# Optimization experiments

Hardware: AMD Instinct MI355X
Metric: run time of the kernel (lower is better)

The kernel has to match this reference:

```python
import jax, jax.numpy as jnp
import numpy as np

D_MODEL = 1024
N_HEADS = 16
HEAD_DIM = D_MODEL // N_HEADS
INNER = 4 * D_MODEL  # mlp_ratio=4
EPS = 1e-5


def setup_inputs() -> dict:
    key = jax.random.key(0)
    ks = jax.random.split(key, 8)
    B, L = 2, 2048
    s = 0.02
    return {
        "x": jax.random.normal(ks[0], (B, L, D_MODEL), dtype=jnp.float32),
        "w_qkv": jax.random.normal(ks[1], (D_MODEL, 3 * D_MODEL), dtype=jnp.float32) * s,
        "b_qkv": jnp.zeros((3 * D_MODEL,), jnp.float32),
        "w_out": jax.random.normal(ks[2], (D_MODEL, D_MODEL), dtype=jnp.float32) * s,
        "b_out": jnp.zeros((D_MODEL,), jnp.float32),
        "w_fc1": jax.random.normal(ks[3], (D_MODEL, INNER), dtype=jnp.float32) * s,
        "b_fc1": jnp.zeros((INNER,), jnp.float32),
        "w_fc2": jax.random.normal(ks[4], (INNER, D_MODEL), dtype=jnp.float32) * s,
        "b_fc2": jnp.zeros((D_MODEL,), jnp.float32),
        "ln1_g": jnp.ones((D_MODEL,), jnp.float32),
        "ln1_b": jnp.zeros((D_MODEL,), jnp.float32),
        "ln2_g": jnp.ones((D_MODEL,), jnp.float32),
        "ln2_b": jnp.zeros((D_MODEL,), jnp.float32),
    }


def _layernorm(x, g, b):
    mu = jnp.mean(x, axis=-1, keepdims=True)
    var = jnp.mean(jnp.square(x - mu), axis=-1, keepdims=True)
    return (x - mu) * jax.lax.rsqrt(var + EPS) * g + b


def reference(x, w_qkv, b_qkv, w_out, b_out, w_fc1, b_fc1, w_fc2, b_fc2,
              ln1_g, ln1_b, ln2_g, ln2_b):
    B, L, D = x.shape
    scale = HEAD_DIM ** -0.5

    # --- attention (prefill, kv_cache=None, S=L) ---
    h = _layernorm(x, ln1_g, ln1_b)
    qkv = (h @ w_qkv + b_qkv).reshape(B, L, 3, N_HEADS, HEAD_DIM)
    q, k, v = (qkv[:, :, i].transpose(0, 2, 1, 3) for i in range(3))  # (B,H,L,hd)
    attn = jnp.einsum('bhqd,bhkd->bhqk', q, k) * scale
    causal = jnp.arange(L)[None, :] > jnp.arange(L)[:, None]  # col > row
    attn = jnp.where(causal[None, None], -jnp.inf, attn)
    attn = jax.nn.softmax(attn, axis=-1)
    o = jnp.einsum('bhqk,bhkd->bhqd', attn, v).transpose(0, 2, 1, 3).reshape(B, L, D)
    x = x + o @ w_out + b_out

    # --- MLP ---
    h2 = _layernorm(x, ln2_g, ln2_b)
    h2 = jax.nn.gelu(h2 @ w_fc1 + b_fc1, approximate=False)  # torch nn.GELU = exact erf
    x = x + h2 @ w_fc2 + b_fc2
    return x
```

## Files before the change

### kernel.cpp

```cpp
#include <hip/hip_runtime.h>
#include <hip/hip_bf16.h>

typedef unsigned short u16;
typedef unsigned int u32;
typedef short bf16x8 __attribute__((ext_vector_type(8)));
typedef float f32x4 __attribute__((ext_vector_type(4)));

#define LOG2E 1.4426950408889634f

#define SEQ 2048
#define DM 1024
#define NH 16
#define HD 64
#define INNER 4096
#define MTOT 4096
#define QKV_ELEMS 4194304

static __device__ __forceinline__ u16 f2bf(float f) {
  u32 u = __float_as_uint(f);
  u = (u + 0x7fffu + ((u >> 16) & 1u)) >> 16;
  return (u16)u;
}

static __device__ __forceinline__ void async_copy16(void* lds, const void* g) {
  __builtin_amdgcn_global_load_lds(
      (const __attribute__((address_space(1))) u32*)g,
      (__attribute__((address_space(3))) u32*)lds, 16, 0, 0);
}

#define MFMA16(a, b, c) __builtin_amdgcn_mfma_f32_16x16x32_bf16(a, b, c, 0, 0, 0)

__global__ __launch_bounds__(256) void transpose_cast(
    const float* __restrict__ src, u16* __restrict__ dst, int K, int N) {
  __shared__ float tile[32][33];
  int bx = blockIdx.x;
  int by = blockIdx.y;
  int t = threadIdx.x;
  int tr = t >> 5, tc = t & 31;
#pragma unroll
  for (int i = 0; i < 4; ++i) {
    int r = by * 32 + tr + i * 8;
    int c = bx * 32 + tc;
    tile[tr + i * 8][tc] = src[(size_t)r * N + c];
  }
  __syncthreads();
#pragma unroll
  for (int i = 0; i < 4; ++i) {
    int n = bx * 32 + tr + i * 8;
    int kk = by * 32 + tc;
    dst[(size_t)n * K + kk] = f2bf(tile[tc][tr + i * 8]);
  }
}

__global__ __launch_bounds__(256) void ln_kernel(
    const float* __restrict__ x, const float* __restrict__ g,
    const float* __restrict__ b, u16* __restrict__ out) {
  int row = blockIdx.x, t = threadIdx.x;
  const float* xr = x + (size_t)row * DM;
  float4 v = *(const float4*)(xr + t * 4);
  float s = v.x + v.y + v.z + v.w;
  float ss = v.x * v.x + v.y * v.y + v.z * v.z + v.w * v.w;
#pragma unroll
  for (int d = 1; d < 64; d <<= 1) {
    s += __shfl_xor(s, d);
    ss += __shfl_xor(ss, d);
  }
  __shared__ float red[8];
  int w = t >> 6, lane = t & 63;
  if (lane == 0) { red[w] = s; red[4 + w] = ss; }
  __syncthreads();
  s = red[0] + red[1] + red[2] + red[3];
  ss = red[4] + red[5] + red[6] + red[7];
  float mu = s * (1.f / DM);
  float var = ss * (1.f / DM) - mu * mu;
  float rstd = rsqrtf(var + 1e-5f);
  float4 gv = *(const float4*)(g + t * 4);
  float4 bv = *(const float4*)(b + t * 4);
  u32 p0 = (u32)f2bf((v.x - mu) * rstd * gv.x + bv.x) |
           ((u32)f2bf((v.y - mu) * rstd * gv.y + bv.y) << 16);
  u32 p1 = (u32)f2bf((v.z - mu) * rstd * gv.z + bv.z) |
           ((u32)f2bf((v.w - mu) * rstd * gv.w + bv.w) << 16);
  uint2 pk; pk.x = p0; pk.y = p1;
  *(uint2*)(out + (size_t)row * DM + t * 4) = pk;
}

template <int EPI>
__global__ __launch_bounds__(256) void gemm_bt(
    const u16* __restrict__ A, const u16* __restrict__ Bt,
    const float* __restrict__ bias, const float* __restrict__ resid,
    void* __restrict__ outp, int M, int N, int K) {
  __shared__ u16 As[128 * 32];
  __shared__ u16 Bs[128 * 32];
  int t = threadIdx.x;
  int lane = t & 63, w = t >> 6;
  int lo = lane & 15, hi = lane >> 4;
  int wr = w >> 1, wc = w & 1;
  int m0 = blockIdx.y * 128, n0 = blockIdx.x * 128;

  f32x4 acc[4][4];
#pragma unroll
  for (int i = 0; i < 4; ++i)
#pragma unroll
    for (int j = 0; j < 4; ++j) acc[i][j] = f32x4{0.f, 0.f, 0.f, 0.f};

  const u16* gA = A + (size_t)(m0 + (t >> 2)) * K + (t & 3) * 8;
  const u16* gB = Bt + (size_t)(n0 + (t >> 2)) * K + (t & 3) * 8;
  char* lA = (char*)As + (t >> 6) * 1024;
  char* lB = (char*)Bs + (t >> 6) * 1024;

  for (int kt = 0; kt < K; kt += 32) {
    async_copy16(lA, gA + kt);
    async_copy16(lA + 4096, gA + (size_t)64 * K + kt);
    async_copy16(lB, gB + kt);
    async_copy16(lB + 4096, gB + (size_t)64 * K + kt);
    __syncthreads();
    bf16x8 af[4], bf[4];
#pragma unroll
    for (int f = 0; f < 4; ++f)
      af[f] = *(const bf16x8*)(As + (wr * 64 + f * 16 + lo) * 32 + hi * 8);
#pragma unroll
    for (int f = 0; f < 4; ++f)
      bf[f] = *(const bf16x8*)(Bs + (wc * 64 + f * 16 + lo) * 32 + hi * 8);
#pragma unroll
    for (int i = 0; i < 4; ++i)
#pragma unroll
      for (int j = 0; j < 4; ++j)
        acc[i][j] = MFMA16(af[i], bf[j], acc[i][j]);
    __syncthreads();
  }

#pragma unroll
  for (int i = 0; i < 4; ++i) {
#pragma unroll
    for (int j = 0; j < 4; ++j) {
      int col = n0 + wc * 64 + j * 16 + lo;
#pragma unroll
      for (int r = 0; r < 4; ++r) {
        int m = m0 + wr * 64 + i * 16 + hi * 4 + r;
        float val = acc[i][j][r];
        if constexpr (EPI == 0) {
          val += bias[col];
          int which = col >> 10;
          int h = (col >> 6) & 15, d = col & 63;
          int b = m >> 11, l = m & 2047;
          size_t bh = (size_t)(b * NH + h);
          u16* qp = (u16*)outp;
          if (which == 0)
            qp[(bh * SEQ + l) * HD + d] = f2bf(val * 0.125f);
          else if (which == 1)
            (qp + QKV_ELEMS)[(bh * SEQ + l) * HD + d] = f2bf(val);
          else
            (qp + 2 * QKV_ELEMS)[(bh * HD + d) * SEQ + l] = f2bf(val);
        } else if constexpr (EPI == 1) {
          val += bias[col] + resid[(size_t)m * N + col];
          ((float*)outp)[(size_t)m * N + col] = val;
        } else {
          val += bias[col];
          val = 0.5f * val * (1.0f + erff(val * 0.7071067811865476f));
          ((u16*)outp)[(size_t)m * N + col] = f2bf(val);
        }
      }
    }
  }
}

__global__ __launch_bounds__(256) void attn_kernel(
    const u16* __restrict__ q, const u16* __restrict__ k,
    const u16* __restrict__ vt, u16* __restrict__ o) {
  int bx = blockIdx.x, bh = blockIdx.y;
  int t = threadIdx.x;
  int lane = t & 63, w = t >> 6;
  int lo = lane & 15, hi = lane >> 4;

  __shared__ u16 Ks[64 * 64];
  __shared__ u16 Vs[64 * 64];
  __shared__ u16 Ps[4][16][72];

  const u16* kg = k + (size_t)bh * SEQ * HD;
  const u16* vg = vt + (size_t)bh * HD * SEQ;
  int b = bh >> 4, h = bh & 15;

  u32 sw = (u32)((lo & 7) << 4);

#pragma unroll 1
  for (int pass = 0; pass < 2; ++pass) {
    int qt = pass == 0 ? (31 - bx) : bx;

    int qrow = qt * 64 + w * 16 + lo;
    const u16* qbase = q + ((size_t)bh * SEQ + qrow) * HD;
    bf16x8 qf0 = *(const bf16x8*)(qbase + hi * 8);
    bf16x8 qf1 = *(const bf16x8*)(qbase + 32 + hi * 8);

    f32x4 o_acc[4];
#pragma unroll
    for (int df = 0; df < 4; ++df) o_acc[df] = f32x4{0.f, 0.f, 0.f, 0.f};
    float m_run[4] = {-INFINITY, -INFINITY, -INFINITY, -INFINITY};
    float s_run[4] = {0.f, 0.f, 0.f, 0.f};

    for (int kt = 0; kt <= qt; ++kt) {
      __syncthreads();
#pragma unroll
      for (int p = 0; p < 2; ++p) {
        int idx = p * 256 + t;
        int r = idx >> 3, c8 = (idx & 7) * 8;
        u32 off = (u32)(r * 128 + c8 * 2);
        u32 soff = off ^ (u32)((r & 7) << 4);
        *(bf16x8*)((char*)Ks + soff) =
            *(const bf16x8*)(kg + ((size_t)(kt * 64 + r)) * HD + c8);
        *(bf16x8*)((char*)Vs + soff) =
            *(const bf16x8*)(vg + (size_t)r * SEQ + kt * 64 + c8);
      }
      __syncthreads();

      f32x4 s[4];
#pragma unroll
      for (int cf = 0; cf < 4; ++cf) {
        s[cf] = f32x4{0.f, 0.f, 0.f, 0.f};
        u32 ro = (u32)((cf * 16 + lo) * 128);
        bf16x8 kf0 = *(const bf16x8*)((char*)Ks + ((ro + hi * 16) ^ sw));
        bf16x8 kf1 = *(const bf16x8*)((char*)Ks + ((ro + 64 + hi * 16) ^ sw));
        s[cf] = MFMA16(qf0, kf0, s[cf]);
        s[cf] = MFMA16(qf1, kf1, s[cf]);
      }

      if (kt == qt) {
#pragma unroll
        for (int cf = 0; cf < 4; ++cf)
#pragma unroll
          for (int r = 0; r < 4; ++r) {
            int kcol = kt * 64 + cf * 16 + lo;
            int qr = qt * 64 + w * 16 + hi * 4 + r;
            if (kcol > qr) s[cf][r] = -INFINITY;
          }
      }

      float alpha[4];
#pragma unroll
      for (int r = 0; r < 4; ++r) {
        float v = fmaxf(fmaxf(s[0][r], s[1][r]), fmaxf(s[2][r], s[3][r]));
        v = fmaxf(v, __shfl_xor(v, 1));
        v = fmaxf(v, __shfl_xor(v, 2));
        v = fmaxf(v, __shfl_xor(v, 4));
        v = fmaxf(v, __shfl_xor(v, 8));
        float mnew = fmaxf(m_run[r], v);
        float a = exp2f((m_run[r] - mnew) * LOG2E);
        m_run[r] = mnew;
        float psum = 0.f;
#pragma unroll
        for (int cf = 0; cf < 4; ++cf) {
          float p = exp2f((s[cf][r] - mnew) * LOG2E);
          Ps[w][hi * 4 + r][cf * 16 + lo] = f2bf(p);
          psum += p;
        }
        psum += __shfl_xor(psum, 1);
        psum += __shfl_xor(psum, 2);
        psum += __shfl_xor(psum, 4);
        psum += __shfl_xor(psum, 8);
        s_run[r] = s_run[r] * a + psum;
        alpha[r] = a;
      }
#pragma unroll
      for (int df = 0; df < 4; ++df)
#pragma unroll
        for (int r = 0; r < 4; ++r) o_acc[df][r] *= alpha[r];

#pragma unroll
      for (int ks = 0; ks < 2; ++ks) {
        bf16x8 pf = *(const bf16x8*)&Ps[w][lo][ks * 32 + hi * 8];
#pragma unroll
        for (int df = 0; df < 4; ++df) {
          u32 ro = (u32)((df * 16 + lo) * 128);
          bf16x8 vf =
              *(const bf16x8*)((char*)Vs + ((ro + ks * 64 + hi * 16) ^ sw));
          o_acc[df] = MFMA16(pf, vf, o_acc[df]);
        }
      }
    }

#pragma unroll
    for (int df = 0; df < 4; ++df) {
#pragma unroll
      for (int r = 0; r < 4; ++r) {
        float val = o_acc[df][r] / s_run[r];
        int orow = qt * 64 + w * 16 + hi * 4 + r;
        size_t oidx = ((size_t)b * SEQ + orow) * DM + h * HD + df * 16 + lo;
        o[oidx] = f2bf(val);
      }
    }
  }
}

extern "C" void kernel_launch(void* const* d_in, const int* in_sizes, int n_in,
                              void* d_out, int out_size, void* d_ws,
                              size_t ws_size, hipStream_t stream) {
  const float* x = (const float*)d_in[0];
  const float* w_qkv = (const float*)d_in[1];
  const float* b_qkv = (const float*)d_in[2];
  const float* w_out = (const float*)d_in[3];
  const float* b_out = (const float*)d_in[4];
  const float* w_fc1 = (const float*)d_in[5];
  const float* b_fc1 = (const float*)d_in[6];
  const float* w_fc2 = (const float*)d_in[7];
  const float* b_fc2 = (const float*)d_in[8];
  const float* ln1_g = (const float*)d_in[9];
  const float* ln1_b = (const float*)d_in[10];
  const float* ln2_g = (const float*)d_in[11];
  const float* ln2_b = (const float*)d_in[12];
  float* out = (float*)d_out;

  char* ws = (char*)d_ws;
  const size_t MB = 1u << 20;
  u16* hb = (u16*)(ws + 0);
  u16* wqkvT = (u16*)(ws + 8 * MB);
  u16* woutT = (u16*)(ws + 14 * MB);
  u16* wfc1T = (u16*)(ws + 16 * MB);
  u16* wfc2T = (u16*)(ws + 24 * MB);
  u16* qb = (u16*)(ws + 32 * MB);
  u16* attn_o = (u16*)(ws + 56 * MB);
  float* x1 = (float*)(ws + 64 * MB);
  u16* gbuf = (u16*)(ws + 32 * MB);

  dim3 blk(256);

  transpose_cast<<<dim3(3072 / 32, 1024 / 32), blk, 0, stream>>>(w_qkv, wqkvT, 1024, 3072);
  transpose_cast<<<dim3(1024 / 32, 1024 / 32), blk, 0, stream>>>(w_out, woutT, 1024, 1024);
  transpose_cast<<<dim3(4096 / 32, 1024 / 32), blk, 0, stream>>>(w_fc1, wfc1T, 1024, 4096);
  transpose_cast<<<dim3(1024 / 32, 4096 / 32), blk, 0, stream>>>(w_fc2, wfc2T, 4096, 1024);

  ln_kernel<<<MTOT, blk, 0, stream>>>(x, ln1_g, ln1_b, hb);

  gemm_bt<0><<<dim3(3072 / 128, MTOT / 128), blk, 0, stream>>>(
      hb, wqkvT, b_qkv, nullptr, qb, MTOT, 3072, 1024);

  attn_kernel<<<dim3(16, 32), blk, 0, stream>>>(
      qb, qb + QKV_ELEMS, qb + 2 * QKV_ELEMS, attn_o);

  gemm_bt<1><<<dim3(1024 / 128, MTOT / 128), blk, 0, stream>>>(
      attn_o, woutT, b_out, x, x1, MTOT, 1024, 1024);

  ln_kernel<<<MTOT, blk, 0, stream>>>(x1, ln2_g, ln2_b, hb);

  gemm_bt<2><<<dim3(4096 / 128, MTOT / 128), blk, 0, stream>>>(
      hb, wfc1T, b_fc1, nullptr, gbuf, MTOT, 4096, 1024);

  gemm_bt<1><<<dim3(1024 / 128, MTOT / 128), blk, 0, stream>>>(
      gbuf, wfc2T, b_fc2, x1, out, MTOT, 1024, 4096);
}
```

Baseline: 469.9 us.

## Double-buffer GEMM LDS tiles, narrow N-tile for D-output GEMMs, fold log2e into Q scale

The GEMM now keeps two LDS buffers and issues the next k-tile's async global-to-LDS loads before computing on the current one, which drops one barrier per iteration and is meant to hide load latency. The GEMM is templated on the N-tile width, and the two GEMMs that produce 1024 output columns use 64-wide tiles so they launch twice as many blocks and fill more CUs. The softmax scale and log2(e) are folded into the Q scaling so attention can call exp2 without an extra multiply. The double buffer doubles LDS use per block, which may lower occupancy.

Result: faster. 430.6 us (-8.4%).

```diff
diff --git a/kernel.cpp b/kernel.cpp
--- a/kernel.cpp
+++ b/kernel.cpp
@@ -5,8 +5,6 @@
 typedef unsigned int u32;
 typedef short bf16x8 __attribute__((ext_vector_type(8)));
 typedef float f32x4 __attribute__((ext_vector_type(4)));
-
-#define LOG2E 1.4426950408889634f
 
 #define SEQ 2048
 #define DM 1024
@@ -84,56 +82,67 @@
   *(uint2*)(out + (size_t)row * DM + t * 4) = pk;
 }
 
-template <int EPI>
+template <int EPI, int BN>
 __global__ __launch_bounds__(256) void gemm_bt(
     const u16* __restrict__ A, const u16* __restrict__ Bt,
     const float* __restrict__ bias, const float* __restrict__ resid,
     void* __restrict__ outp, int M, int N, int K) {
-  __shared__ u16 As[128 * 32];
-  __shared__ u16 Bs[128 * 32];
+  constexpr int NF = BN / 32;
+  __shared__ u16 As[2][128 * 32];
+  __shared__ u16 Bs[2][BN * 32];
   int t = threadIdx.x;
   int lane = t & 63, w = t >> 6;
   int lo = lane & 15, hi = lane >> 4;
   int wr = w >> 1, wc = w & 1;
-  int m0 = blockIdx.y * 128, n0 = blockIdx.x * 128;
-
-  f32x4 acc[4][4];
+  int m0 = blockIdx.y * 128, n0 = blockIdx.x * BN;
+
+  f32x4 acc[4][NF];
 #pragma unroll
   for (int i = 0; i < 4; ++i)
 #pragma unroll
-    for (int j = 0; j < 4; ++j) acc[i][j] = f32x4{0.f, 0.f, 0.f, 0.f};
+    for (int j = 0; j < NF; ++j) acc[i][j] = f32x4{0.f, 0.f, 0.f, 0.f};
 
   const u16* gA = A + (size_t)(m0 + (t >> 2)) * K + (t & 3) * 8;
   const u16* gB = Bt + (size_t)(n0 + (t >> 2)) * K + (t & 3) * 8;
-  char* lA = (char*)As + (t >> 6) * 1024;
-  char* lB = (char*)Bs + (t >> 6) * 1024;
-
-  for (int kt = 0; kt < K; kt += 32) {
-    async_copy16(lA, gA + kt);
-    async_copy16(lA + 4096, gA + (size_t)64 * K + kt);
-    async_copy16(lB, gB + kt);
-    async_copy16(lB + 4096, gB + (size_t)64 * K + kt);
+
+  auto STAGE = [&](int buf, int kt) {
+    char* lA = (char*)(&As[buf][0]) + w * 1024;
+    char* lB = (char*)(&Bs[buf][0]) + w * 1024;
+    async_copy16(lA, gA + kt * 32);
+    async_copy16(lA + 4096, gA + (size_t)64 * K + kt * 32);
+    async_copy16(lB, gB + kt * 32);
+    if constexpr (BN == 128)
+      async_copy16(lB + 4096, gB + (size_t)64 * K + kt * 32);
+  };
+
+  int nk = K >> 5;
+  int buf = 0;
+  STAGE(0, 0);
+  __syncthreads();
+
+  for (int kt = 0; kt < nk; ++kt) {
+    if (kt + 1 < nk) STAGE(buf ^ 1, kt + 1);
+    bf16x8 af[4], bq[NF];
+#pragma unroll
+    for (int f = 0; f < 4; ++f)
+      af[f] = *(const bf16x8*)(&As[buf][(wr * 64 + f * 16 + lo) * 32 + hi * 8]);
+#pragma unroll
+    for (int j = 0; j < NF; ++j)
+      bq[j] = *(const bf16x8*)(&Bs[buf][(wc * (BN / 2) + j * 16 + lo) * 32 + hi * 8]);
+#pragma unroll
+    for (int i = 0; i < 4; ++i)
+#pragma unroll
+      for (int j = 0; j < NF; ++j)
+        acc[i][j] = MFMA16(af[i], bq[j], acc[i][j]);
     __syncthreads();
-    bf16x8 af[4], bf[4];
-#pragma unroll
-    for (int f = 0; f < 4; ++f)
-      af[f] = *(const bf16x8*)(As + (wr * 64 + f * 16 + lo) * 32 + hi * 8);
-#pragma unroll
-    for (int f = 0; f < 4; ++f)
-      bf[f] = *(const bf16x8*)(Bs + (wc * 64 + f * 16 + lo) * 32 + hi * 8);
-#pragma unroll
-    for (int i = 0; i < 4; ++i)
-#pragma unroll
-      for (int j = 0; j < 4; ++j)
-        acc[i][j] = MFMA16(af[i], bf[j], acc[i][j]);
-    __syncthreads();
+    buf ^= 1;
   }
 
 #pragma unroll
   for (int i = 0; i < 4; ++i) {
 #pragma unroll
-    for (int j = 0; j < 4; ++j) {
-      int col = n0 + wc * 64 + j * 16 + lo;
+    for (int j = 0; j < NF; ++j) {
+      int col = n0 + wc * (BN / 2) + j * 16 + lo;
 #pragma unroll
       for (int r = 0; r < 4; ++r) {
         int m = m0 + wr * 64 + i * 16 + hi * 4 + r;
@@ -146,7 +155,7 @@
           size_t bh = (size_t)(b * NH + h);
           u16* qp = (u16*)outp;
           if (which == 0)
-            qp[(bh * SEQ + l) * HD + d] = f2bf(val * 0.125f);
+            qp[(bh * SEQ + l) * HD + d] = f2bf(val * 0.18033688011112043f);
           else if (which == 1)
             (qp + QKV_ELEMS)[(bh * SEQ + l) * HD + d] = f2bf(val);
           else
@@ -243,12 +252,12 @@
         v = fmaxf(v, __shfl_xor(v, 4));
         v = fmaxf(v, __shfl_xor(v, 8));
         float mnew = fmaxf(m_run[r], v);
-        float a = exp2f((m_run[r] - mnew) * LOG2E);
+        float a = exp2f(m_run[r] - mnew);
         m_run[r] = mnew;
         float psum = 0.f;
 #pragma unroll
         for (int cf = 0; cf < 4; ++cf) {
-          float p = exp2f((s[cf][r] - mnew) * LOG2E);
+          float p = exp2f(s[cf][r] - mnew);
           Ps[w][hi * 4 + r][cf * 16 + lo] = f2bf(p);
           psum += p;
         }
@@ -329,20 +338,20 @@
 
   ln_kernel<<<MTOT, blk, 0, stream>>>(x, ln1_g, ln1_b, hb);
 
-  gemm_bt<0><<<dim3(3072 / 128, MTOT / 128), blk, 0, stream>>>(
+  gemm_bt<0, 128><<<dim3(3072 / 128, MTOT / 128), blk, 0, stream>>>(
       hb, wqkvT, b_qkv, nullptr, qb, MTOT, 3072, 1024);
 
   attn_kernel<<<dim3(16, 32), blk, 0, stream>>>(
       qb, qb + QKV_ELEMS, qb + 2 * QKV_ELEMS, attn_o);
 
-  gemm_bt<1><<<dim3(1024 / 128, MTOT / 128), blk, 0, stream>>>(
+  gemm_bt<1, 64><<<dim3(1024 / 64, MTOT / 128), blk, 0, stream>>>(
       attn_o, woutT, b_out, x, x1, MTOT, 1024, 1024);
 
   ln_kernel<<<MTOT, blk, 0, stream>>>(x1, ln2_g, ln2_b, hb);
 
-  gemm_bt<2><<<dim3(4096 / 128, MTOT / 128), blk, 0, stream>>>(
+  gemm_bt<2, 128><<<dim3(4096 / 128, MTOT / 128), blk, 0, stream>>>(
       hb, wfc1T, b_fc1, nullptr, gbuf, MTOT, 4096, 1024);
 
-  gemm_bt<1><<<dim3(1024 / 128, MTOT / 128), blk, 0, stream>>>(
+  gemm_bt<1, 64><<<dim3(1024 / 64, MTOT / 128), blk, 0, stream>>>(
       gbuf, wfc2T, b_fc2, x1, out, MTOT, 1024, 4096);
 }
```
